# Kernel optimization log

Measured on AMD Instinct MI355X. Metric: run time of the kernel, lower is better.

## Reference

```python
import jax, jax.numpy as jnp
import numpy as np

N_NODES = 100000
N_EDGES = 1600000
IN_DIM = 64
OUT_DIM = 64


def setup_inputs() -> dict:
    key = jax.random.key(0)
    k1, k2, k3, k4 = jax.random.split(key, 4)
    x = jax.random.normal(k1, (N_NODES, IN_DIM), dtype=jnp.float32)
    edge_index = jax.random.randint(k2, (2, N_EDGES), 0, N_NODES, dtype=jnp.int64)
    # nn.Linear-style init: U(-1/sqrt(in), 1/sqrt(in))
    lim = 1.0 / np.sqrt(IN_DIM)
    W = jax.random.uniform(k3, (OUT_DIM, IN_DIM), dtype=jnp.float32, minval=-lim, maxval=lim)
    b = jax.random.uniform(k4, (OUT_DIM,), dtype=jnp.float32, minval=-lim, maxval=lim)
    return {"x": x, "edge_index": edge_index, "W": W, "b": b}


def reference(x, edge_index, W, b):
    n = x.shape[0]
    row, col = edge_index[0], edge_index[1]
    # gather source features along edges, scatter-add into destination rows
    agg = jax.ops.segment_sum(x[col], row, num_segments=n)  # [n, in_dim]
    deg = jax.ops.segment_sum(jnp.ones(row.shape[0], dtype=x.dtype), row, num_segments=n)
    deg = jnp.clip(deg, 1.0, None)[:, None]  # [n, 1]
    out = agg / deg
    return out @ W.T + b  # [n, out_dim]
```

## Files before the change

kernel.cpp:

```cpp
#include <hip/hip_runtime.h>
#include <hip/hip_bf16.h>
#include <hip/hip_fp16.h>

#define DIM 64
#define NPART 8

typedef _Float16 half2_t __attribute__((ext_vector_type(2)));

#if defined(__has_builtin)
#if __has_builtin(__builtin_amdgcn_fdot2)
#define HAVE_FDOT2 1
#endif
#endif

__device__ __forceinline__ float dot2acc(unsigned int mu, unsigned int wu, float acc) {
#ifdef HAVE_FDOT2
    return __builtin_amdgcn_fdot2(__builtin_bit_cast(half2_t, mu),
                                  __builtin_bit_cast(half2_t, wu), acc, false);
#else
    const float2 mf = __half22float2(*(const __half2*)&mu);
    const float2 wf = __half22float2(*(const __half2*)&wu);
    return acc + mf.x * wf.x + mf.y * wf.y;
#endif
}

__global__ void __launch_bounds__(256) setup_kernel(
    const float4* __restrict__ x, ushort4* __restrict__ xh4,
    const float2* __restrict__ W2, unsigned int* __restrict__ wh2,
    int* __restrict__ cnt, int* __restrict__ partTot, int* __restrict__ bumpP,
    int n4, int n) {
    const int i = blockIdx.x * 256 + threadIdx.x;
    if (i < n4) {
        const float4 v = x[i];
        ushort4 o;
        o.x = __half_as_ushort(__float2half(v.x));
        o.y = __half_as_ushort(__float2half(v.y));
        o.z = __half_as_ushort(__float2half(v.z));
        o.w = __half_as_ushort(__float2half(v.w));
        xh4[i] = o;
    }
    if (i < DIM * DIM / 2) {
        const float2 f = W2[i];
        const __half2 h = __floats2half2_rn(f.x, f.y);
        wh2[i] = *(const unsigned int*)&h;
    }
    if (i < (n >> 2)) ((int4*)cnt)[i] = make_int4(0, 0, 0, 0);
    if (i == 0) for (int k = n & ~3; k < n; ++k) cnt[k] = 0;
    if (i < NPART) { partTot[i] = 0; bumpP[i] = 0; }
}

__global__ void __launch_bounds__(256) prep_bin_kernel(
    const void* __restrict__ eiv, int* __restrict__ cnt,
    uint2* __restrict__ bins, int* __restrict__ binCnt,
    int nE, int bound, int cap) {
    __shared__ int lcnt[NPART], lbase[NPART], sIs64;
    const int tid = threadIdx.x;
    if (tid < NPART) lcnt[tid] = 0;
    if (tid < 64) {
        const unsigned int hi = ((const unsigned int*)eiv)[2 * tid + 1];
        const unsigned long long ball = __ballot(hi != 0u);
        if (tid == 0) sIs64 = (ball == 0ULL) ? 1 : 0;
    }
    __syncthreads();
    const int is64 = sIs64;
    const int base = (blockIdx.x * 256 + tid) * 4;
    int r[4], c[4], pp[4], off[4];
    int nv = 0;
    if (base < nE) {
        nv = nE - base; if (nv > 4) nv = 4;
        if (nv == 4 && (nE & 3) == 0) {
            if (is64) {
                const long long* ei = (const long long*)eiv;
                const longlong2 r01 = *(const longlong2*)&ei[base];
                const longlong2 r23 = *(const longlong2*)&ei[base + 2];
                const longlong2 c01 = *(const longlong2*)&ei[nE + base];
                const longlong2 c23 = *(const longlong2*)&ei[nE + base + 2];
                r[0] = (int)r01.x; r[1] = (int)r01.y; r[2] = (int)r23.x; r[3] = (int)r23.y;
                c[0] = (int)c01.x; c[1] = (int)c01.y; c[2] = (int)c23.x; c[3] = (int)c23.y;
            } else {
                const int* ei = (const int*)eiv;
                const int4 rr = *(const int4*)&ei[base];
                const int4 cc = *(const int4*)&ei[nE + base];
                r[0] = rr.x; r[1] = rr.y; r[2] = rr.z; r[3] = rr.w;
                c[0] = cc.x; c[1] = cc.y; c[2] = cc.z; c[3] = cc.w;
            }
        } else {
            for (int k = 0; k < nv; ++k) {
                if (is64) {
                    const long long* ei = (const long long*)eiv;
                    r[k] = (int)ei[base + k]; c[k] = (int)ei[nE + base + k];
                } else {
                    const int* ei = (const int*)eiv;
                    r[k] = ei[base + k]; c[k] = ei[nE + base + k];
                }
            }
        }
    }
    #pragma unroll
    for (int k = 0; k < 4; ++k) {
        if (k < nv) {
            int p = r[k] / bound; if (p > NPART - 1) p = NPART - 1;
            pp[k] = p;
            off[k] = atomicAdd(&lcnt[p], 1);
            atomicAdd(&cnt[r[k]], 1);
        }
    }
    __syncthreads();
    if (tid < NPART) lbase[tid] = atomicAdd(&binCnt[tid], lcnt[tid]);
    __syncthreads();
    #pragma unroll
    for (int k = 0; k < 4; ++k) {
        if (k < nv) {
            const int idx = lbase[pp[k]] + off[k];
            if (idx < cap)
                bins[(size_t)pp[k] * cap + idx] = make_uint2((unsigned)r[k], (unsigned)c[k]);
        }
    }
}

__global__ void __launch_bounds__(256) prep32_kernel(
    const void* __restrict__ eiv, int* __restrict__ rows32, int* __restrict__ cols32,
    int* __restrict__ cnt, int* __restrict__ partTot, int nE, int bound) {
    __shared__ int lcnt[NPART], sIs64;
    const int tid = threadIdx.x;
    if (tid < NPART) lcnt[tid] = 0;
    if (tid < 64) {
        const unsigned int hi = ((const unsigned int*)eiv)[2 * tid + 1];
        const unsigned long long ball = __ballot(hi != 0u);
        if (tid == 0) sIs64 = (ball == 0ULL) ? 1 : 0;
    }
    __syncthreads();
    const int is64 = sIs64;
    const int base = (blockIdx.x * 256 + tid) * 4;
    int r[4], c[4];
    int nv = 0;
    if (base < nE) {
        nv = nE - base; if (nv > 4) nv = 4;
        if (nv == 4 && (nE & 3) == 0) {
            if (is64) {
                const long long* ei = (const long long*)eiv;
                const longlong2 r01 = *(const longlong2*)&ei[base];
                const longlong2 r23 = *(const longlong2*)&ei[base + 2];
                const longlong2 c01 = *(const longlong2*)&ei[nE + base];
                const longlong2 c23 = *(const longlong2*)&ei[nE + base + 2];
                r[0] = (int)r01.x; r[1] = (int)r01.y; r[2] = (int)r23.x; r[3] = (int)r23.y;
                c[0] = (int)c01.x; c[1] = (int)c01.y; c[2] = (int)c23.x; c[3] = (int)c23.y;
            } else {
                const int* ei = (const int*)eiv;
                const int4 rr = *(const int4*)&ei[base];
                const int4 cc = *(const int4*)&ei[nE + base];
                r[0] = rr.x; r[1] = rr.y; r[2] = rr.z; r[3] = rr.w;
                c[0] = cc.x; c[1] = cc.y; c[2] = cc.z; c[3] = cc.w;
            }
            *(int4*)&rows32[base] = make_int4(r[0], r[1], r[2], r[3]);
            *(int4*)&cols32[base] = make_int4(c[0], c[1], c[2], c[3]);
        } else {
            for (int k = 0; k < nv; ++k) {
                if (is64) {
                    const long long* ei = (const long long*)eiv;
                    r[k] = (int)ei[base + k]; c[k] = (int)ei[nE + base + k];
                } else {
                    const int* ei = (const int*)eiv;
                    r[k] = ei[base + k]; c[k] = ei[nE + base + k];
                }
                rows32[base + k] = r[k]; cols32[base + k] = c[k];
            }
        }
    }
    #pragma unroll
    for (int k = 0; k < 4; ++k) {
        if (k < nv) {
            int p = r[k] / bound; if (p > NPART - 1) p = NPART - 1;
            atomicAdd(&lcnt[p], 1);
            atomicAdd(&cnt[r[k]], 1);
        }
    }
    __syncthreads();
    if (tid < NPART && lcnt[tid] > 0) atomicAdd(&partTot[tid], lcnt[tid]);
}

__global__ void __launch_bounds__(256) alloc_kernel(
    const int* __restrict__ cnt, int* __restrict__ cursor,
    const int* __restrict__ partTot, int* __restrict__ bumpP, int n, int bound) {
    const int gid  = blockIdx.x * 256 + threadIdx.x;
    const int lane = threadIdx.x & 63;
    const bool act = gid < n;
    const int v = act ? cnt[gid] : 0;
    int inc = v;
    #pragma unroll
    for (int off = 1; off < 64; off <<= 1) {
        const int t = __shfl_up(inc, off);
        if (lane >= off) inc += t;
    }
    const int total = __shfl(inc, 63);
    const int excl  = inc - v;
    const int rr = act ? gid : (n - 1);
    int p = rr / bound; if (p > NPART - 1) p = NPART - 1;
    p = __builtin_amdgcn_readfirstlane(p);
    int wbase = 0;
    if (lane == 0) {
        int pb = 0;
        for (int q = 0; q < p; ++q) pb += partTot[q];
        wbase = pb + atomicAdd(&bumpP[p], total);
    }
    wbase = __shfl(wbase, 0);
    if (act) cursor[gid] = wbase + excl;
}

__global__ void __launch_bounds__(256) build_bin_kernel(
    const uint2* __restrict__ bins, const int* __restrict__ binCnt,
    int* __restrict__ cursor, int* __restrict__ scol, int cap) {
    const int p = blockIdx.x & (NPART - 1);
    const int m = binCnt[p];
    const int start  = (blockIdx.x >> 3) * 256 + threadIdx.x;
    const int stride = (gridDim.x >> 3) * 256;
    for (int i = start; i < m; i += stride) {
        const uint2 rc = bins[(size_t)p * cap + i];
        const int pos = atomicAdd(&cursor[rc.x], 1);
        scol[pos] = (int)rc.y;
    }
}

__global__ void __launch_bounds__(256) build_part32_kernel(
    const int* __restrict__ rows32, const int* __restrict__ cols32,
    int* __restrict__ cursor, int* __restrict__ scol, int nE, int bound) {
    const int p  = blockIdx.x & (NPART - 1);
    const int q  = blockIdx.x / NPART;
    const int nq = gridDim.x / NPART;
    const unsigned lo = (unsigned)p * (unsigned)bound;
    const unsigned bnd = (unsigned)((p == NPART - 1) ? 0x7fffffff : bound);
    const int stride = nq * 256;
    for (int e = q * 256 + (int)threadIdx.x; e < nE; e += stride) {
        const int r = rows32[e];
        if ((unsigned)r - lo < bnd) {
            const int pos = atomicAdd(&cursor[r], 1);
            scol[pos] = cols32[e];
        }
    }
}

__global__ void __launch_bounds__(256) gather_finalize_q_kernel(
    const __half* __restrict__ xh, const int* __restrict__ scol,
    const int* __restrict__ cursor, const int* __restrict__ cnt,
    const unsigned int* __restrict__ wh2, const float* __restrict__ b,
    float* __restrict__ out, int n) {
    __shared__ __align__(16) unsigned int rowh[4][32];
    const int tid   = threadIdx.x;
    const int group = tid >> 6;
    const int lane  = tid & 63;
    const int q     = lane >> 4;
    const int s16   = lane & 15;
    const int wid   = (int)((blockIdx.x * 256 + tid) >> 6);
    const int nw    = (int)((gridDim.x * 256) >> 6);

    unsigned int wcu[32];
    #pragma unroll
    for (int i = 0; i < 32; ++i) wcu[i] = wh2[lane * 32 + i];
    #pragma unroll
    for (int i = 0; i < 32; ++i) asm volatile("" : "+v"(wcu[i]));

    const float bl = b[lane];

    for (int r0 = wid; r0 < n; r0 += nw) {
        const int r   = __builtin_amdgcn_readfirstlane(r0);
        const int k   = cnt[r];
        const int end = cursor[r];
        const int s   = end - k;
        float a0 = 0.f, a1 = 0.f, a2 = 0.f, a3 = 0.f;
        int j = 0;
        for (; j + 15 < k; j += 16) {
            const int cA = scol[s + j + q];
            const int cB = scol[s + j + 4 + q];
            const int cC = scol[s + j + 8 + q];
            const int cD = scol[s + j + 12 + q];
            const uint2 uA = *(const uint2*)(xh + ((size_t)cA << 6) + (s16 << 2));
            const uint2 uB = *(const uint2*)(xh + ((size_t)cB << 6) + (s16 << 2));
            const uint2 uC = *(const uint2*)(xh + ((size_t)cC << 6) + (s16 << 2));
            const uint2 uD = *(const uint2*)(xh + ((size_t)cD << 6) + (s16 << 2));
            float2 f;
            f = __half22float2(*(const __half2*)&uA.x); a0 += f.x; a1 += f.y;
            f = __half22float2(*(const __half2*)&uA.y); a2 += f.x; a3 += f.y;
            f = __half22float2(*(const __half2*)&uB.x); a0 += f.x; a1 += f.y;
            f = __half22float2(*(const __half2*)&uB.y); a2 += f.x; a3 += f.y;
            f = __half22float2(*(const __half2*)&uC.x); a0 += f.x; a1 += f.y;
            f = __half22float2(*(const __half2*)&uC.y); a2 += f.x; a3 += f.y;
            f = __half22float2(*(const __half2*)&uD.x); a0 += f.x; a1 += f.y;
            f = __half22float2(*(const __half2*)&uD.y); a2 += f.x; a3 += f.y;
        }
        for (; j + 7 < k; j += 8) {
            const int cA = scol[s + j + q];
            const int cB = scol[s + j + 4 + q];
            const uint2 uA = *(const uint2*)(xh + ((size_t)cA << 6) + (s16 << 2));
            const uint2 uB = *(const uint2*)(xh + ((size_t)cB << 6) + (s16 << 2));
            float2 f;
            f = __half22float2(*(const __half2*)&uA.x); a0 += f.x; a1 += f.y;
            f = __half22float2(*(const __half2*)&uA.y); a2 += f.x; a3 += f.y;
            f = __half22float2(*(const __half2*)&uB.x); a0 += f.x; a1 += f.y;
            f = __half22float2(*(const __half2*)&uB.y); a2 += f.x; a3 += f.y;
        }
        if (j + 3 < k) {
            const int cA = scol[s + j + q];
            const uint2 uA = *(const uint2*)(xh + ((size_t)cA << 6) + (s16 << 2));
            float2 f;
            f = __half22float2(*(const __half2*)&uA.x); a0 += f.x; a1 += f.y;
            f = __half22float2(*(const __half2*)&uA.y); a2 += f.x; a3 += f.y;
            j += 4;
        }
        for (; j < k; ++j) {
            const int c = scol[s + j];
            if (q == 0) {
                const uint2 u = *(const uint2*)(xh + ((size_t)c << 6) + (s16 << 2));
                float2 f;
                f = __half22float2(*(const __half2*)&u.x); a0 += f.x; a1 += f.y;
                f = __half22float2(*(const __half2*)&u.y); a2 += f.x; a3 += f.y;
            }
        }
        a0 += __shfl_xor(a0, 16); a0 += __shfl_xor(a0, 32);
        a1 += __shfl_xor(a1, 16); a1 += __shfl_xor(a1, 32);
        a2 += __shfl_xor(a2, 16); a2 += __shfl_xor(a2, 32);
        a3 += __shfl_xor(a3, 16); a3 += __shfl_xor(a3, 32);
        const float inv = 1.0f / ((k > 0) ? (float)k : 1.0f);
        if (q == 0) {
            const __half2 m01 = __floats2half2_rn(a0 * inv, a1 * inv);
            const __half2 m23 = __floats2half2_rn(a2 * inv, a3 * inv);
            uint2 mu;
            mu.x = *(const unsigned int*)&m01;
            mu.y = *(const unsigned int*)&m23;
            *(uint2*)&rowh[group][s16 * 2] = mu;
        }
        float dot = bl;
        #pragma unroll
        for (int i4 = 0; i4 < 8; ++i4) {
            const uint4 mm = *(const uint4*)&rowh[group][i4 * 4];
            dot = dot2acc(mm.x, wcu[i4 * 4 + 0], dot);
            dot = dot2acc(mm.y, wcu[i4 * 4 + 1], dot);
            dot = dot2acc(mm.z, wcu[i4 * 4 + 2], dot);
            dot = dot2acc(mm.w, wcu[i4 * 4 + 3], dot);
        }
        out[(size_t)r * DIM + lane] = dot;
    }
}

extern "C" void kernel_launch(void* const* d_in, const int* in_sizes, int n_in,
                              void* d_out, int out_size, void* d_ws, size_t ws_size,
                              hipStream_t stream) {
    const float* x  = (const float*)d_in[0];
    const void*  ei = (const void*)d_in[1];
    const float* W  = (const float*)d_in[2];
    const float* b  = (const float*)d_in[3];
    float* out = (float*)d_out;

    const int n  = in_sizes[0] / DIM;
    const int nE = in_sizes[1] / 2;

    const int bound = (((n + NPART - 1) / NPART) + 63) & ~63;
    const int cap   = ((nE + NPART - 1) / NPART) * 3 / 2 + 256;

    const int scolPad = (nE + 3) & ~3;
    int* wsI     = (int*)d_ws;
    int* cnt     = wsI;
    int* cursor  = wsI + n;
    int* partTot = wsI + 2 * n;
    int* bumpP   = wsI + 2 * n + 8;
    int* scol    = wsI + 2 * n + 64;
    __half* xh   = (__half*)(scol + scolPad);
    unsigned int* wh2 = (unsigned int*)(xh + (size_t)n * DIM);
    uint2* bins  = (uint2*)(wh2 + 2048);
    int* rows32  = (int*)(wh2 + 2048);
    int* cols32  = rows32 + nE;

    const size_t base_ints = (size_t)2 * n + 64 + scolPad + (size_t)n * (DIM / 2) + 2048;
    const size_t need_A = (base_ints + (size_t)2 * NPART * cap) * sizeof(int);
    const size_t need_B = (base_ints + (size_t)2 * nE) * sizeof(int);

    const int n4 = n * DIM / 4;
    int maxi = n4;
    if (maxi < DIM * DIM / 2) maxi = DIM * DIM / 2;
    if (maxi < (n + 3) / 4) maxi = (n + 3) / 4;

    if (ws_size >= need_A) {
        setup_kernel<<<(maxi + 255) / 256, 256, 0, stream>>>(
            (const float4*)x, (ushort4*)xh, (const float2*)W, wh2,
            cnt, partTot, bumpP, n4, n);
        prep_bin_kernel<<<(nE + 1023) / 1024, 256, 0, stream>>>(
            ei, cnt, bins, partTot, nE, bound, cap);
        alloc_kernel<<<(n + 255) / 256, 256, 0, stream>>>(
            cnt, cursor, partTot, bumpP, n, bound);
        build_bin_kernel<<<2048, 256, 0, stream>>>(bins, partTot, cursor, scol, cap);
        gather_finalize_q_kernel<<<2048, 256, 0, stream>>>(
            xh, scol, cursor, cnt, wh2, b, out, n);
    } else if (ws_size >= need_B) {
        setup_kernel<<<(maxi + 255) / 256, 256, 0, stream>>>(
            (const float4*)x, (ushort4*)xh, (const float2*)W, wh2,
            cnt, partTot, bumpP, n4, n);
        prep32_kernel<<<(nE + 1023) / 1024, 256, 0, stream>>>(
            ei, rows32, cols32, cnt, partTot, nE, bound);
        alloc_kernel<<<(n + 255) / 256, 256, 0, stream>>>(
            cnt, cursor, partTot, bumpP, n, bound);
        build_part32_kernel<<<2048, 256, 0, stream>>>(rows32, cols32, cursor, scol, nE, bound);
        gather_finalize_q_kernel<<<2048, 256, 0, stream>>>(
            xh, scol, cursor, cnt, wh2, b, out, n);
    }
}
```

Baseline: 318.5 us.

## Replicate partition bins and rank edges with wave ballots instead of LDS atomics

The edge-binning kernel now computes each edge's slot inside its partition with per-wave ballot and popcount ranking. One lane per partition does a single global atomic, which replaces the LDS atomics and the two block barriers. Bin counters are split into REP sub-bins per partition, chosen by block index, to spread contention on the global counters. The alloc and build kernels iterate over the sub-bins. This adds more bin-capacity slack and makes the build loop visit more bins.

```diff
diff --git a/kernel.cpp b/kernel.cpp
--- a/kernel.cpp
+++ b/kernel.cpp
@@ -4,6 +4,7 @@
 
 #define DIM 64
 #define NPART 8
+#define REP 8
 
 typedef _Float16 half2_t __attribute__((ext_vector_type(2)));
 
@@ -27,8 +28,7 @@
 __global__ void __launch_bounds__(256) setup_kernel(
     const float4* __restrict__ x, ushort4* __restrict__ xh4,
     const float2* __restrict__ W2, unsigned int* __restrict__ wh2,
-    int* __restrict__ cnt, int* __restrict__ partTot, int* __restrict__ bumpP,
-    int n4, int n) {
+    int* __restrict__ cnt, int* __restrict__ ctrs, int n4, int n) {
     const int i = blockIdx.x * 256 + threadIdx.x;
     if (i < n4) {
         const float4 v = x[i];
@@ -46,16 +46,15 @@
     }
     if (i < (n >> 2)) ((int4*)cnt)[i] = make_int4(0, 0, 0, 0);
     if (i == 0) for (int k = n & ~3; k < n; ++k) cnt[k] = 0;
-    if (i < NPART) { partTot[i] = 0; bumpP[i] = 0; }
-}
-
-__global__ void __launch_bounds__(256) prep_bin_kernel(
+    if (i < 32) ((int4*)ctrs)[i] = make_int4(0, 0, 0, 0);
+}
+
+__global__ void __launch_bounds__(256) prep_ms_kernel(
     const void* __restrict__ eiv, int* __restrict__ cnt,
     uint2* __restrict__ bins, int* __restrict__ binCnt,
-    int nE, int bound, int cap) {
-    __shared__ int lcnt[NPART], lbase[NPART], sIs64;
+    int nE, int bound, int subcap) {
+    __shared__ int sIs64;
     const int tid = threadIdx.x;
-    if (tid < NPART) lcnt[tid] = 0;
     if (tid < 64) {
         const unsigned int hi = ((const unsigned int*)eiv)[2 * tid + 1];
         const unsigned long long ball = __ballot(hi != 0u);
@@ -63,57 +62,81 @@
     }
     __syncthreads();
     const int is64 = sIs64;
+    const int lane = tid & 63;
+    const unsigned long long below = (1ULL << lane) - 1ULL;
+    const int rep  = blockIdx.x & (REP - 1);
     const int base = (blockIdx.x * 256 + tid) * 4;
-    int r[4], c[4], pp[4], off[4];
-    int nv = 0;
-    if (base < nE) {
-        nv = nE - base; if (nv > 4) nv = 4;
-        if (nv == 4 && (nE & 3) == 0) {
+    int nv = nE - base; nv = nv < 0 ? 0 : (nv > 4 ? 4 : nv);
+
+    int r[4] = {0, 0, 0, 0}, c[4] = {0, 0, 0, 0};
+    if (nv == 4) {
+        if (is64) {
+            const long long* ei = (const long long*)eiv;
+            const longlong2 r01 = *(const longlong2*)&ei[base];
+            const longlong2 r23 = *(const longlong2*)&ei[base + 2];
+            const longlong2 c01 = *(const longlong2*)&ei[nE + base];
+            const longlong2 c23 = *(const longlong2*)&ei[nE + base + 2];
+            r[0] = (int)r01.x; r[1] = (int)r01.y; r[2] = (int)r23.x; r[3] = (int)r23.y;
+            c[0] = (int)c01.x; c[1] = (int)c01.y; c[2] = (int)c23.x; c[3] = (int)c23.y;
+        } else {
+            const int* ei = (const int*)eiv;
+            const int4 rr = *(const int4*)&ei[base];
+            const int4 cc = *(const int4*)&ei[nE + base];
+            r[0] = rr.x; r[1] = rr.y; r[2] = rr.z; r[3] = rr.w;
+            c[0] = cc.x; c[1] = cc.y; c[2] = cc.z; c[3] = cc.w;
+        }
+    } else if (nv > 0) {
+        for (int k = 0; k < nv; ++k) {
             if (is64) {
                 const long long* ei = (const long long*)eiv;
-                const longlong2 r01 = *(const longlong2*)&ei[base];
-                const longlong2 r23 = *(const longlong2*)&ei[base + 2];
-                const longlong2 c01 = *(const longlong2*)&ei[nE + base];
-                const longlong2 c23 = *(const longlong2*)&ei[nE + base + 2];
-                r[0] = (int)r01.x; r[1] = (int)r01.y; r[2] = (int)r23.x; r[3] = (int)r23.y;
-                c[0] = (int)c01.x; c[1] = (int)c01.y; c[2] = (int)c23.x; c[3] = (int)c23.y;
+                r[k] = (int)ei[base + k]; c[k] = (int)ei[nE + base + k];
             } else {
                 const int* ei = (const int*)eiv;
-                const int4 rr = *(const int4*)&ei[base];
-                const int4 cc = *(const int4*)&ei[nE + base];
-                r[0] = rr.x; r[1] = rr.y; r[2] = rr.z; r[3] = rr.w;
-                c[0] = cc.x; c[1] = cc.y; c[2] = cc.z; c[3] = cc.w;
+                r[k] = ei[base + k]; c[k] = ei[nE + base + k];
             }
-        } else {
-            for (int k = 0; k < nv; ++k) {
-                if (is64) {
-                    const long long* ei = (const long long*)eiv;
-                    r[k] = (int)ei[base + k]; c[k] = (int)ei[nE + base + k];
-                } else {
-                    const int* ei = (const int*)eiv;
-                    r[k] = ei[base + k]; c[k] = ei[nE + base + k];
-                }
-            }
-        }
-    }
+        }
+    }
+
+    int pp[4], rank[4], myCnt[4];
+    #pragma unroll
+    for (int k = 0; k < 4; ++k) {
+        const bool valid = k < nv;
+        int p = r[k] / bound; if (p > NPART - 1) p = NPART - 1;
+        if (!valid) p = 0;
+        pp[k] = p;
+        const unsigned long long vm = __ballot(valid);
+        const unsigned long long m0 = __ballot(valid && (p & 1));
+        const unsigned long long m1 = __ballot(valid && (p & 2));
+        const unsigned long long m2 = __ballot(valid && (p & 4));
+        const unsigned long long s =
+            vm & ((p & 1) ? m0 : ~m0) & ((p & 2) ? m1 : ~m1) & ((p & 4) ? m2 : ~m2);
+        rank[k] = (int)__popcll(s & below);
+        const int i = lane;
+        const unsigned long long si =
+            vm & ((i & 1) ? m0 : ~m0) & ((i & 2) ? m1 : ~m1) & ((i & 4) ? m2 : ~m2);
+        myCnt[k] = (int)__popcll(si);
+    }
+    const int pre0 = 0;
+    const int pre1 = myCnt[0];
+    const int pre2 = pre1 + myCnt[1];
+    const int pre3 = pre2 + myCnt[2];
+    const int tot  = pre3 + myCnt[3];
+    int wbase = 0;
+    if (lane < NPART && tot > 0)
+        wbase = atomicAdd(&binCnt[lane * REP + rep], tot);
+    int bb[4];
+    bb[0] = __shfl(wbase + pre0, pp[0]);
+    bb[1] = __shfl(wbase + pre1, pp[1]);
+    bb[2] = __shfl(wbase + pre2, pp[2]);
+    bb[3] = __shfl(wbase + pre3, pp[3]);
     #pragma unroll
     for (int k = 0; k < 4; ++k) {
         if (k < nv) {
-            int p = r[k] / bound; if (p > NPART - 1) p = NPART - 1;
-            pp[k] = p;
-            off[k] = atomicAdd(&lcnt[p], 1);
+            const int idx = bb[k] + rank[k];
+            if (idx < subcap)
+                bins[(size_t)(pp[k] * REP + rep) * subcap + idx] =
+                    make_uint2((unsigned)r[k], (unsigned)c[k]);
             atomicAdd(&cnt[r[k]], 1);
-        }
-    }
-    __syncthreads();
-    if (tid < NPART) lbase[tid] = atomicAdd(&binCnt[tid], lcnt[tid]);
-    __syncthreads();
-    #pragma unroll
-    for (int k = 0; k < 4; ++k) {
-        if (k < nv) {
-            const int idx = lbase[pp[k]] + off[k];
-            if (idx < cap)
-                bins[(size_t)pp[k] * cap + idx] = make_uint2((unsigned)r[k], (unsigned)c[k]);
         }
     }
 }
@@ -136,7 +159,7 @@
     int nv = 0;
     if (base < nE) {
         nv = nE - base; if (nv > 4) nv = 4;
-        if (nv == 4 && (nE & 3) == 0) {
+        if (nv == 4) {
             if (is64) {
                 const long long* ei = (const long long*)eiv;
                 const longlong2 r01 = *(const longlong2*)&ei[base];
@@ -181,7 +204,8 @@
 
 __global__ void __launch_bounds__(256) alloc_kernel(
     const int* __restrict__ cnt, int* __restrict__ cursor,
-    const int* __restrict__ partTot, int* __restrict__ bumpP, int n, int bound) {
+    const int* __restrict__ pt, int ptStride, int* __restrict__ bumpP,
+    int n, int bound) {
     const int gid  = blockIdx.x * 256 + threadIdx.x;
     const int lane = threadIdx.x & 63;
     const bool act = gid < n;
@@ -200,7 +224,8 @@
     int wbase = 0;
     if (lane == 0) {
         int pb = 0;
-        for (int q = 0; q < p; ++q) pb += partTot[q];
+        for (int q = 0; q < p; ++q)
+            for (int j = 0; j < ptStride; ++j) pb += pt[q * ptStride + j];
         wbase = pb + atomicAdd(&bumpP[p], total);
     }
     wbase = __shfl(wbase, 0);
@@ -209,15 +234,19 @@
 
 __global__ void __launch_bounds__(256) build_bin_kernel(
     const uint2* __restrict__ bins, const int* __restrict__ binCnt,
-    int* __restrict__ cursor, int* __restrict__ scol, int cap) {
-    const int p = blockIdx.x & (NPART - 1);
-    const int m = binCnt[p];
-    const int start  = (blockIdx.x >> 3) * 256 + threadIdx.x;
-    const int stride = (gridDim.x >> 3) * 256;
-    for (int i = start; i < m; i += stride) {
-        const uint2 rc = bins[(size_t)p * cap + i];
-        const int pos = atomicAdd(&cursor[rc.x], 1);
-        scol[pos] = (int)rc.y;
+    int* __restrict__ cursor, int* __restrict__ scol, int subcap) {
+    const int p  = blockIdx.x & (NPART - 1);
+    const int bq = blockIdx.x >> 3;
+    const int nb = gridDim.x >> 3;
+    for (int rep = 0; rep < REP; ++rep) {
+        int m = binCnt[p * REP + rep];
+        if (m > subcap) m = subcap;
+        const uint2* bp = bins + (size_t)(p * REP + rep) * subcap;
+        for (int i = bq * 256 + (int)threadIdx.x; i < m; i += nb * 256) {
+            const uint2 rc = bp[i];
+            const int pos = atomicAdd(&cursor[rc.x], 1);
+            scol[pos] = (int)rc.y;
+        }
     }
 }
 
@@ -353,24 +382,26 @@
     const int n  = in_sizes[0] / DIM;
     const int nE = in_sizes[1] / 2;
 
-    const int bound = (((n + NPART - 1) / NPART) + 63) & ~63;
-    const int cap   = ((nE + NPART - 1) / NPART) * 3 / 2 + 256;
+    const int bound  = (((n + NPART - 1) / NPART) + 63) & ~63;
+    const int subcap = (((nE / (NPART * REP)) * 3) / 2 + 256) & ~1;
 
     const int scolPad = (nE + 3) & ~3;
     int* wsI     = (int*)d_ws;
     int* cnt     = wsI;
     int* cursor  = wsI + n;
-    int* partTot = wsI + 2 * n;
-    int* bumpP   = wsI + 2 * n + 8;
-    int* scol    = wsI + 2 * n + 64;
+    int* ctrs    = wsI + 2 * n;
+    int* binCnt  = ctrs;
+    int* bumpP   = ctrs + 64;
+    int* partTot = ctrs + 72;
+    int* scol    = wsI + 2 * n + 128;
     __half* xh   = (__half*)(scol + scolPad);
     unsigned int* wh2 = (unsigned int*)(xh + (size_t)n * DIM);
     uint2* bins  = (uint2*)(wh2 + 2048);
     int* rows32  = (int*)(wh2 + 2048);
     int* cols32  = rows32 + nE;
 
-    const size_t base_ints = (size_t)2 * n + 64 + scolPad + (size_t)n * (DIM / 2) + 2048;
-    const size_t need_A = (base_ints + (size_t)2 * NPART * cap) * sizeof(int);
+    const size_t base_ints = (size_t)2 * n + 128 + scolPad + (size_t)n * (DIM / 2) + 2048;
+    const size_t need_A = (base_ints + (size_t)2 * NPART * REP * subcap) * sizeof(int);
     const size_t need_B = (base_ints + (size_t)2 * nE) * sizeof(int);
 
     const int n4 = n * DIM / 4;
@@ -380,23 +411,21 @@
 
     if (ws_size >= need_A) {
         setup_kernel<<<(maxi + 255) / 256, 256, 0, stream>>>(
-            (const float4*)x, (ushort4*)xh, (const float2*)W, wh2,
-            cnt, partTot, bumpP, n4, n);
-        prep_bin_kernel<<<(nE + 1023) / 1024, 256, 0, stream>>>(
-            ei, cnt, bins, partTot, nE, bound, cap);
+            (const float4*)x, (ushort4*)xh, (const float2*)W, wh2, cnt, ctrs, n4, n);
+        prep_ms_kernel<<<(nE + 1023) / 1024, 256, 0, stream>>>(
+            ei, cnt, bins, binCnt, nE, bound, subcap);
         alloc_kernel<<<(n + 255) / 256, 256, 0, stream>>>(
-            cnt, cursor, partTot, bumpP, n, bound);
-        build_bin_kernel<<<2048, 256, 0, stream>>>(bins, partTot, cursor, scol, cap);
+            cnt, cursor, binCnt, REP, bumpP, n, bound);
+        build_bin_kernel<<<2048, 256, 0, stream>>>(bins, binCnt, cursor, scol, subcap);
         gather_finalize_q_kernel<<<2048, 256, 0, stream>>>(
             xh, scol, cursor, cnt, wh2, b, out, n);
     } else if (ws_size >= need_B) {
         setup_kernel<<<(maxi + 255) / 256, 256, 0, stream>>>(
-            (const float4*)x, (ushort4*)xh, (const float2*)W, wh2,
-            cnt, partTot, bumpP, n4, n);
+            (const float4*)x, (ushort4*)xh, (const float2*)W, wh2, cnt, ctrs, n4, n);
         prep32_kernel<<<(nE + 1023) / 1024, 256, 0, stream>>>(
             ei, rows32, cols32, cnt, partTot, nE, bound);
         alloc_kernel<<<(n + 255) / 256, 256, 0, stream>>>(
-            cnt, cursor, partTot, bumpP, n, bound);
+            cnt, cursor, partTot, 1, bumpP, n, bound);
         build_part32_kernel<<<2048, 256, 0, stream>>>(rows32, cols32, cursor, scol, nE, bound);
         gather_finalize_q_kernel<<<2048, 256, 0, stream>>>(
             xh, scol, cursor, cnt, wh2, b, out, n);
```

Result: slower. 422.3 us (+32.6%).
